# Kernel tuning notes

Measured on AMD Instinct MI355X. Metric: run time of the kernel, lower is better.

The kernel has to match this reference:

```python
import jax, jax.numpy as jnp
import numpy as np

H = 128  # hidden_dim
COORD_CLAMP = 100.0


def _glorot(key, shape):
    fan_in, fan_out = shape[0], shape[1]
    lim = float(np.sqrt(6.0 / (fan_in + fan_out)))
    return jax.random.uniform(key, shape, jnp.float32, -lim, lim)


def setup_inputs() -> dict:
    key = jax.random.key(0)
    ks = jax.random.split(key, 20)
    B, N = 2, 512
    inp = {
        "h": jax.random.normal(ks[0], (B, N, H), jnp.float32),
        "pos": jax.random.normal(ks[1], (B, N, 3), jnp.float32),
        "vel": jax.random.normal(ks[2], (B, N, 3), jnp.float32),
        # edge_mlp: Linear(2H+2 -> H), SiLU, Linear(H -> H), SiLU
        "We1": _glorot(ks[3], (2 * H + 2, H)), "be1": jnp.zeros((H,), jnp.float32),
        "We2": _glorot(ks[4], (H, H)), "be2": jnp.zeros((H,), jnp.float32),
        # attention_mlp: Linear(H -> 1), Sigmoid
        "Wa": _glorot(ks[5], (H, 1)), "ba": jnp.zeros((1,), jnp.float32),
        # pos_mlp: Linear(H -> H), SiLU, Linear(H -> 1, no bias)
        "Wp1": _glorot(ks[6], (H, H)), "bp1": jnp.zeros((H,), jnp.float32),
        "Wp2": _glorot(ks[7], (H, 1)),
        # vel_mlp: Linear(H -> H), SiLU, Linear(H -> 1, no bias)
        "Wv1": _glorot(ks[8], (H, H)), "bv1": jnp.zeros((H,), jnp.float32),
        "Wv2": _glorot(ks[9], (H, 1)),
        # node_mlp: Linear(2H -> H), SiLU, Linear(H -> H)
        "Wn1": _glorot(ks[10], (2 * H, H)), "bn1": jnp.zeros((H,), jnp.float32),
        "Wn2": _glorot(ks[11], (H, H)), "bn2": jnp.zeros((H,), jnp.float32),
    }
    return inp


def reference(h, pos, vel, We1, be1, We2, be2, Wa, ba,
              Wp1, bp1, Wp2, Wv1, bv1, Wv2, Wn1, bn1, Wn2, bn2):
    B, N, _ = pos.shape
    # pairwise diffs: [B, N, N, 3]
    pos_diff = pos[:, :, None, :] - pos[:, None, :, :]
    vel_diff = vel[:, :, None, :] - vel[:, None, :, :]
    pos_dist_sq = jnp.sum(pos_diff ** 2, axis=-1, keepdims=True)  # [B,N,N,1]
    vel_dist_sq = jnp.sum(vel_diff ** 2, axis=-1, keepdims=True)
    h_i = jnp.broadcast_to(h[:, :, None, :], (B, N, N, H))
    h_j = jnp.broadcast_to(h[:, None, :, :], (B, N, N, H))
    edge_input = jnp.concatenate([h_i, h_j, pos_dist_sq, vel_dist_sq], axis=-1)  # [B,N,N,2H+2]
    # edge MLP
    m = jax.nn.silu(jnp.einsum('bijc,ch->bijh', edge_input, We1) + be1)
    m_ij = jax.nn.silu(jnp.einsum('bijh,hk->bijk', m, We2) + be2)
    # attention gate
    att = jax.nn.sigmoid(jnp.einsum('bijh,ho->bijo', m_ij, Wa) + ba)  # [B,N,N,1]
    m_ij = m_ij * att
    # tanh-weighted coordinate/velocity updates
    pos_w = jnp.tanh(jnp.einsum('bijh,ho->bijo', jax.nn.silu(jnp.einsum('bijh,hk->bijk', m_ij, Wp1) + bp1), Wp2))
    vel_w = jnp.tanh(jnp.einsum('bijh,ho->bijo', jax.nn.silu(jnp.einsum('bijh,hk->bijk', m_ij, Wv1) + bv1), Wv2))
    denom = jnp.float32(max(N - 1, 1))
    pos_update = jnp.sum(pos_diff * pos_w, axis=2) / denom  # [B,N,3]
    vel_update = jnp.sum(vel_diff * vel_w, axis=2) / denom
    pos_out = jnp.clip(pos + pos_update, -COORD_CLAMP, COORD_CLAMP)
    vel_out = jnp.clip(vel + vel_update, -COORD_CLAMP, COORD_CLAMP)
    # node update
    m_agg = jnp.sum(m_ij, axis=2)  # [B,N,H]
    node_input = jnp.concatenate([h, m_agg], axis=-1)  # [B,N,2H]
    h_out = jax.nn.silu(jnp.einsum('bnc,ch->bnh', node_input, Wn1) + bn1)
    h_out = jnp.einsum('bnh,hk->bnk', h_out, Wn2) + bn2
    h_out = h + h_out  # residual
    return (h_out, pos_out, vel_out)
```

## Files before the change

kernel.cpp:

```cpp
#include <hip/hip_runtime.h>
#include <hip/hip_bf16.h>

#define Hd 128
#define Nn 512
#define TJ 32
#define LSTRIDE 136

typedef __bf16 bf16x8 __attribute__((ext_vector_type(8)));
typedef __bf16 bf16x4 __attribute__((ext_vector_type(4)));
typedef float  floatx4 __attribute__((ext_vector_type(4)));

__device__ __forceinline__ float frcp(float x){ return __builtin_amdgcn_rcpf(x); }
__device__ __forceinline__ float fsilu(float x){ return x * frcp(1.f + __expf(-x)); }
__device__ __forceinline__ float fsigm(float x){ return frcp(1.f + __expf(-x)); }
__device__ __forceinline__ float ftanh(float x){ return 1.f - 2.f * frcp(__expf(2.f*x) + 1.f); }
__device__ __forceinline__ float rfl(float x){
  return __int_as_float(__builtin_amdgcn_readfirstlane(__float_as_int(x)));
}

__global__ __launch_bounds__(256) void prep(const float* __restrict__ h,
                                            const float* __restrict__ We1,
                                            const float* __restrict__ be1,
                                            const float* __restrict__ We2,
                                            const float* __restrict__ Wp1,
                                            const float* __restrict__ Wv1,
                                            float* __restrict__ A,
                                            float* __restrict__ Bm,
                                            __bf16* __restrict__ dst,
                                            float* __restrict__ zbase){
  if (blockIdx.x < 256){
    const int r0 = blockIdx.x * 4;
    const int k = threadIdx.x & 127, ch = threadIdx.x >> 7;
    __shared__ float hL[4][Hd];
    __shared__ float pa[2][4][Hd], pb[2][4][Hd];
    for (int idx = threadIdx.x; idx < 4*Hd; idx += 256)
      hL[idx >> 7][idx & 127] = h[r0*Hd + idx];
    __syncthreads();
    float a[4] = {0.f,0.f,0.f,0.f}, bb[4] = {0.f,0.f,0.f,0.f};
    const int cbase = ch*64;
    #pragma unroll 4
    for (int cc = 0; cc < 64; ++cc){
      const int c = cbase + cc;
      const float wa = We1[c*Hd + k];
      const float wb = We1[(c + Hd)*Hd + k];
      #pragma unroll
      for (int rr = 0; rr < 4; ++rr){
        a[rr]  += hL[rr][c] * wa;
        bb[rr] += hL[rr][c] * wb;
      }
    }
    #pragma unroll
    for (int rr = 0; rr < 4; ++rr){ pa[ch][rr][k] = a[rr]; pb[ch][rr][k] = bb[rr]; }
    __syncthreads();
    if (threadIdx.x < Hd){
      const float be = be1[k];
      #pragma unroll
      for (int rr = 0; rr < 4; ++rr){
        A[(r0+rr)*Hd + k]  = pa[0][rr][k] + pa[1][rr][k] + be;
        Bm[(r0+rr)*Hd + k] = pb[0][rr][k] + pb[1][rr][k];
      }
    }
  } else if (blockIdx.x < 280){
    const int blk = blockIdx.x - 256;
    const int which = blk >> 3, m = blk & 7;
    const float* src = (which == 0) ? We2 : (which == 1 ? Wp1 : Wv1);
    __bf16* d = dst + which * (Hd*Hd);
    #pragma unroll
    for (int it = 0; it < 8; ++it){
      const int sidx = m*2048 + it*256 + threadIdx.x;
      const int kk = sidx >> 7, cc = sidx & 127;
      const int s = kk >> 5, j = kk & 7;
      const int lane = ((kk >> 3) & 3)*16 + (cc & 15);
      const int n = cc >> 4;
      d[n*2048 + s*512 + lane*8 + j] = (__bf16)src[sidx];
    }
  } else {
    const int t0 = (blockIdx.x - 280)*256 + threadIdx.x;
    for (int idx = t0; idx < 137216; idx += 2048) zbase[idx] = 0.f;
  }
}

__global__ __launch_bounds__(256) void egnn_bf(
    const float* __restrict__ h,
    const float* __restrict__ pos, const float* __restrict__ vel,
    const float* __restrict__ We1, const float* __restrict__ be2,
    const float* __restrict__ Wa,  const float* __restrict__ ba,
    const float* __restrict__ bp1, const float* __restrict__ Wp2,
    const float* __restrict__ bv1, const float* __restrict__ Wv2,
    const float* __restrict__ Wn1, const float* __restrict__ bn1,
    const float* __restrict__ Wn2, const float* __restrict__ bn2,
    const float* __restrict__ A,   const float* __restrict__ Bm,
    const __bf16* __restrict__ Wsw,
    float* __restrict__ out){

  const int t    = threadIdx.x;
  const int w    = t >> 6;
  const int lane = t & 63;
  const int q    = lane >> 4;
  const int l15  = lane & 15;
  const int node = blockIdx.x;
  const int b    = node >> 9;

  __shared__ float AiL[Hd], wpL[Hd], wvL[Hd];
  __shared__ float be2L[Hd], bp1L[Hd], bv1L[Hd], WaL[Hd], Wp2L[Hd], Wv2L[Hd];
  __shared__ __align__(16) __bf16 bufij[4*32*LSTRIDE];
  __shared__ float attW[4][32];

  if (t < Hd){
    AiL[t]  = A[(size_t)node*Hd + t];
    wpL[t]  = We1[256*Hd + t];
    wvL[t]  = We1[257*Hd + t];
    be2L[t] = be2[t]; bp1L[t] = bp1[t]; bv1L[t] = bv1[t];
    WaL[t]  = Wa[t];  Wp2L[t] = Wp2[t]; Wv2L[t] = Wv2[t];
  }
  const float baV = ba[0];
  const float* pi = &pos[(size_t)node*3];
  const float* vi = &vel[(size_t)node*3];
  const float px = rfl(pi[0]), py = rfl(pi[1]), pz = rfl(pi[2]);
  const float ux = rfl(vi[0]), uy = rfl(vi[1]), uz = rfl(vi[2]);
  __syncthreads();

  const bf16x8* We2s = (const bf16x8*)(Wsw);
  const bf16x8* Wp1s = (const bf16x8*)(Wsw + Hd*Hd);
  const bf16x8* Wv1s = (const bf16x8*)(Wsw + 2*Hd*Hd);
  __bf16* myBuf = &bufij[w*32*LSTRIDE];
  float*  myAtt = attW[w];

  float accP0=0.f, accP1=0.f, accP2=0.f, accV0=0.f, accV1=0.f, accV2=0.f;
  float acc8[8];
  #pragma unroll
  for (int e = 0; e < 8; ++e) acc8[e] = 0.f;

  const floatx4 fzero = {0.f,0.f,0.f,0.f};

  #pragma unroll 1
  for (int jt = 0; jt < 4; ++jt){
    const int j0 = w*128 + jt*32;
    const size_t row0 = (size_t)(b*Nn + j0 + l15);
    const size_t row1 = row0 + 16;

    float dp[2], dv[2];
    {
      const float* pj0 = &pos[row0*3]; const float* vj0 = &vel[row0*3];
      const float* pj1 = &pos[row1*3]; const float* vj1 = &vel[row1*3];
      float dx = px - pj0[0], dy = py - pj0[1], dz = pz - pj0[2];
      dp[0] = dx*dx + dy*dy + dz*dz;
      dx = px - pj1[0]; dy = py - pj1[1]; dz = pz - pj1[2];
      dp[1] = dx*dx + dy*dy + dz*dz;
      float ex = ux - vj0[0], ey = uy - vj0[1], ez = uz - vj0[2];
      dv[0] = ex*ex + ey*ey + ez*ez;
      ex = ux - vj1[0]; ey = uy - vj1[1]; ez = uz - vj1[2];
      dv[1] = ex*ex + ey*ey + ez*ez;
    }

    bf16x8 mf[4][2];
    #pragma unroll
    for (int s = 0; s < 4; ++s){
      const int fo = s*32 + q*8;
      const floatx4 A0 = *(const floatx4*)&AiL[fo], A1 = *(const floatx4*)&AiL[fo+4];
      const floatx4 P0 = *(const floatx4*)&wpL[fo], P1 = *(const floatx4*)&wpL[fo+4];
      const floatx4 V0 = *(const floatx4*)&wvL[fo], V1 = *(const floatx4*)&wvL[fo+4];
      #pragma unroll
      for (int n = 0; n < 2; ++n){
        const floatx4* Bp = (const floatx4*)&Bm[(n ? row1 : row0)*Hd + fo];
        const floatx4 b0 = Bp[0], b1 = Bp[1];
        float x[8];
        #pragma unroll
        for (int e = 0; e < 4; ++e){
          x[e]   = fsilu(A0[e] + b0[e] + dp[n]*P0[e] + dv[n]*V0[e]);
          x[4+e] = fsilu(A1[e] + b1[e] + dp[n]*P1[e] + dv[n]*V1[e]);
        }
        union { bf16x8 v; __hip_bfloat162 h2[4]; } o;
        o.h2[0] = __float22bfloat162_rn(make_float2(x[0], x[1]));
        o.h2[1] = __float22bfloat162_rn(make_float2(x[2], x[3]));
        o.h2[2] = __float22bfloat162_rn(make_float2(x[4], x[5]));
        o.h2[3] = __float22bfloat162_rn(make_float2(x[6], x[7]));
        mf[s][n] = o.v;
      }
    }

    float aw0 = 0.f, aw1 = 0.f;
    #pragma unroll
    for (int f = 0; f < 2; ++f){
      floatx4 acc[4][2];
      #pragma unroll
      for (int m4 = 0; m4 < 4; ++m4){ acc[m4][0] = fzero; acc[m4][1] = fzero; }
      #pragma unroll
      for (int s = 0; s < 4; ++s){
        #pragma unroll
        for (int m4 = 0; m4 < 4; ++m4){
          const bf16x8 a = We2s[((f*4 + m4)*4 + s)*64 + lane];
          acc[m4][0] = __builtin_amdgcn_mfma_f32_16x16x32_bf16(a, mf[s][0], acc[m4][0], 0, 0, 0);
          acc[m4][1] = __builtin_amdgcn_mfma_f32_16x16x32_bf16(a, mf[s][1], acc[m4][1], 0, 0, 0);
        }
      }
      #pragma unroll
      for (int m4 = 0; m4 < 4; ++m4){
        const int fb = (f*4 + m4)*16 + q*4;
        const floatx4 be = *(const floatx4*)&be2L[fb];
        const floatx4 wa = *(const floatx4*)&WaL[fb];
        float s0[4], s1[4];
        #pragma unroll
        for (int r = 0; r < 4; ++r){
          s0[r] = fsilu(acc[m4][0][r] + be[r]);
          s1[r] = fsilu(acc[m4][1][r] + be[r]);
          aw0 += s0[r]*wa[r];
          aw1 += s1[r]*wa[r];
        }
        union { bf16x4 v; __hip_bfloat162 h2[2]; } k0, k1;
        k0.h2[0] = __float22bfloat162_rn(make_float2(s0[0], s0[1]));
        k0.h2[1] = __float22bfloat162_rn(make_float2(s0[2], s0[3]));
        k1.h2[0] = __float22bfloat162_rn(make_float2(s1[0], s1[1]));
        k1.h2[1] = __float22bfloat162_rn(make_float2(s1[2], s1[3]));
        *(bf16x4*)&myBuf[l15*LSTRIDE + fb]        = k0.v;
        *(bf16x4*)&myBuf[(16 + l15)*LSTRIDE + fb] = k1.v;
      }
    }
    aw0 += __shfl_xor(aw0, 16, 64); aw0 += __shfl_xor(aw0, 32, 64);
    aw1 += __shfl_xor(aw1, 16, 64); aw1 += __shfl_xor(aw1, 32, 64);
    const float att0 = fsigm(aw0 + baV);
    const float att1 = fsigm(aw1 + baV);
    if (lane < 16){ myAtt[l15] = att0; myAtt[16 + l15] = att1; }

    {
      float p0 = 0.f, p1 = 0.f;
      #pragma unroll
      for (int f = 0; f < 2; ++f){
        floatx4 acc[4][2];
        #pragma unroll
        for (int m4 = 0; m4 < 4; ++m4){ acc[m4][0] = fzero; acc[m4][1] = fzero; }
        #pragma unroll
        for (int s = 0; s < 4; ++s){
          const bf16x8 b0 = *(const bf16x8*)&myBuf[l15*LSTRIDE + s*32 + q*8];
          const bf16x8 b1 = *(const bf16x8*)&myBuf[(16 + l15)*LSTRIDE + s*32 + q*8];
          #pragma unroll
          for (int m4 = 0; m4 < 4; ++m4){
            const bf16x8 a = Wp1s[((f*4 + m4)*4 + s)*64 + lane];
            acc[m4][0] = __builtin_amdgcn_mfma_f32_16x16x32_bf16(a, b0, acc[m4][0], 0, 0, 0);
            acc[m4][1] = __builtin_amdgcn_mfma_f32_16x16x32_bf16(a, b1, acc[m4][1], 0, 0, 0);
          }
        }
        #pragma unroll
        for (int m4 = 0; m4 < 4; ++m4){
          const int fb = (f*4 + m4)*16 + q*4;
          const floatx4 bb = *(const floatx4*)&bp1L[fb];
          const floatx4 w2 = *(const floatx4*)&Wp2L[fb];
          #pragma unroll
          for (int r = 0; r < 4; ++r){
            p0 += fsilu(fmaf(att0, acc[m4][0][r], bb[r])) * w2[r];
            p1 += fsilu(fmaf(att1, acc[m4][1][r], bb[r])) * w2[r];
          }
        }
      }
      p0 += __shfl_xor(p0, 16, 64); p0 += __shfl_xor(p0, 32, 64);
      p1 += __shfl_xor(p1, 16, 64); p1 += __shfl_xor(p1, 32, 64);
      const float pw0 = ftanh(p0), pw1 = ftanh(p1);
      const float* pj0 = &pos[row0*3];
      const float* pj1 = &pos[row1*3];
      accP0 += (px - pj0[0])*pw0 + (px - pj1[0])*pw1;
      accP1 += (py - pj0[1])*pw0 + (py - pj1[1])*pw1;
      accP2 += (pz - pj0[2])*pw0 + (pz - pj1[2])*pw1;
    }

    {
      float p0 = 0.f, p1 = 0.f;
      #pragma unroll
      for (int f = 0; f < 2; ++f){
        floatx4 acc[4][2];
        #pragma unroll
        for (int m4 = 0; m4 < 4; ++m4){ acc[m4][0] = fzero; acc[m4][1] = fzero; }
        #pragma unroll
        for (int s = 0; s < 4; ++s){
          const bf16x8 b0 = *(const bf16x8*)&myBuf[l15*LSTRIDE + s*32 + q*8];
          const bf16x8 b1 = *(const bf16x8*)&myBuf[(16 + l15)*LSTRIDE + s*32 + q*8];
          #pragma unroll
          for (int m4 = 0; m4 < 4; ++m4){
            const bf16x8 a = Wv1s[((f*4 + m4)*4 + s)*64 + lane];
            acc[m4][0] = __builtin_amdgcn_mfma_f32_16x16x32_bf16(a, b0, acc[m4][0], 0, 0, 0);
            acc[m4][1] = __builtin_amdgcn_mfma_f32_16x16x32_bf16(a, b1, acc[m4][1], 0, 0, 0);
          }
        }
        #pragma unroll
        for (int m4 = 0; m4 < 4; ++m4){
          const int fb = (f*4 + m4)*16 + q*4;
          const floatx4 bb = *(const floatx4*)&bv1L[fb];
          const floatx4 w2 = *(const floatx4*)&Wv2L[fb];
          #pragma unroll
          for (int r = 0; r < 4; ++r){
            p0 += fsilu(fmaf(att0, acc[m4][0][r], bb[r])) * w2[r];
            p1 += fsilu(fmaf(att1, acc[m4][1][r], bb[r])) * w2[r];
          }
        }
      }
      p0 += __shfl_xor(p0, 16, 64); p0 += __shfl_xor(p0, 32, 64);
      p1 += __shfl_xor(p1, 16, 64); p1 += __shfl_xor(p1, 32, 64);
      const float vw0 = ftanh(p0), vw1 = ftanh(p1);
      const float* vj0 = &vel[row0*3];
      const float* vj1 = &vel[row1*3];
      accV0 += (ux - vj0[0])*vw0 + (ux - vj1[0])*vw1;
      accV1 += (uy - vj0[1])*vw0 + (uy - vj1[1])*vw1;
      accV2 += (uz - vj0[2])*vw0 + (uz - vj1[2])*vw1;
    }

    {
      const int fg = lane & 15, jr = lane >> 4;
      #pragma unroll
      for (int k = 0; k < 8; ++k){
        const int jl = jr*8 + k;
        const float aj = myAtt[jl];
        const bf16x8 v = *(const bf16x8*)&myBuf[jl*LSTRIDE + fg*8];
        #pragma unroll
        for (int e = 0; e < 8; ++e) acc8[e] += aj * (float)v[e];
      }
    }
  }

  float* sMagW = (float*)myBuf;
  float* sPVW  = (float*)myBuf + 128;
  {
    float r6[6] = {accP0, accP1, accP2, accV0, accV1, accV2};
    #pragma unroll
    for (int off = 1; off < 64; off <<= 1){
      #pragma unroll
      for (int e = 0; e < 6; ++e) r6[e] += __shfl_xor(r6[e], off, 64);
    }
    if (lane == 0){
      #pragma unroll
      for (int e = 0; e < 6; ++e) sPVW[e] = r6[e];
    }
    #pragma unroll
    for (int e = 0; e < 8; ++e){
      acc8[e] += __shfl_xor(acc8[e], 16, 64);
      acc8[e] += __shfl_xor(acc8[e], 32, 64);
    }
    if (lane < 16){
      *(float4*)&sMagW[l15*8 + 0] = make_float4(acc8[0], acc8[1], acc8[2], acc8[3]);
      *(float4*)&sMagW[l15*8 + 4] = make_float4(acc8[4], acc8[5], acc8[6], acc8[7]);
    }
  }
  __syncthreads();

  float* sF = (float*)bufij + 1024;
  {
    const float* s0 = (const float*)(bufij);
    const float* s1 = (const float*)(bufij + 32*LSTRIDE);
    const float* s2 = (const float*)(bufij + 64*LSTRIDE);
    const float* s3 = (const float*)(bufij + 96*LSTRIDE);
    if (t < Hd){
      sF[128 + t] = s0[t] + s1[t] + s2[t] + s3[t];
      sF[t] = h[(size_t)node*Hd + t];
    } else if (t < Hd + 3){
      const int d = t - Hd;
      const float v = 0.25f*(s0[128+d] + s1[128+d] + s2[128+d] + s3[128+d]);
      const float o = pi[d] + v*(1.f/511.f);
      out[2*Nn*Hd + node*3 + d] = fminf(fmaxf(o, -100.f), 100.f);
    } else if (t < Hd + 6){
      const int d = t - Hd - 3;
      const float v = 0.25f*(s0[131+d] + s1[131+d] + s2[131+d] + s3[131+d]);
      const float o = vi[d] + v*(1.f/511.f);
      out[2*Nn*Hd + 2*Nn*3 + node*3 + d] = fminf(fmaxf(o, -100.f), 100.f);
    }
  }
  __syncthreads();
  {
    const int k = t & 127, ch = t >> 7;
    const int cb = ch*Hd;
    float a0=0.f,a1=0.f,a2=0.f,a3=0.f;
    #pragma unroll 8
    for (int cc = 0; cc < Hd; cc += 4){
      a0 += sF[cb+cc+0] * Wn1[(cb+cc+0)*Hd + k];
      a1 += sF[cb+cc+1] * Wn1[(cb+cc+1)*Hd + k];
      a2 += sF[cb+cc+2] * Wn1[(cb+cc+2)*Hd + k];
      a3 += sF[cb+cc+3] * Wn1[(cb+cc+3)*Hd + k];
    }
    sF[256 + ch*128 + k] = (a0+a1)+(a2+a3);
  }
  __syncthreads();
  if (t < Hd) sF[512 + t] = fsilu(sF[256 + t] + sF[384 + t] + bn1[t]);
  __syncthreads();
  {
    const int k = t & 127, ch = t >> 7;
    const int cb = ch*64;
    float a0=0.f,a1=0.f,a2=0.f,a3=0.f;
    #pragma unroll 8
    for (int cc = 0; cc < 64; cc += 4){
      a0 += sF[512+cb+cc+0] * Wn2[(cb+cc+0)*Hd + k];
      a1 += sF[512+cb+cc+1] * Wn2[(cb+cc+1)*Hd + k];
      a2 += sF[512+cb+cc+2] * Wn2[(cb+cc+2)*Hd + k];
      a3 += sF[512+cb+cc+3] * Wn2[(cb+cc+3)*Hd + k];
    }
    sF[256 + ch*128 + k] = (a0+a1)+(a2+a3);
  }
  __syncthreads();
  if (t < Hd)
    out[(size_t)node*Hd + t] = sF[t] + sF[256 + t] + sF[384 + t] + bn2[t];
}

__device__ __forceinline__ void gemm_kloopT(const __bf16* __restrict__ buf,
                                            const bf16x8* __restrict__ Ws,
                                            int w, int lane, int q, int l15,
                                            floatx4 acc[2][2]){
  const floatx4 zero = {0.f, 0.f, 0.f, 0.f};
  #pragma unroll
  for (int m = 0; m < 2; ++m){ acc[m][0] = zero; acc[m][1] = zero; }
  #pragma unroll
  for (int s = 0; s < 4; ++s){
    bf16x8 bf[2];
    #pragma unroll
    for (int n = 0; n < 2; ++n)
      bf[n] = *(const bf16x8*)&buf[(16*n + l15)*LSTRIDE + s*32 + q*8];
    const bf16x8 a0 = Ws[((2*w + 0)*4 + s)*64 + lane];
    const bf16x8 a1 = Ws[((2*w + 1)*4 + s)*64 + lane];
    #pragma unroll
    for (int n = 0; n < 2; ++n){
      acc[0][n] = __builtin_amdgcn_mfma_f32_16x16x32_bf16(a0, bf[n], acc[0][n], 0, 0, 0);
      acc[1][n] = __builtin_amdgcn_mfma_f32_16x16x32_bf16(a1, bf[n], acc[1][n], 0, 0, 0);
    }
  }
}

__device__ __forceinline__ void wdotT(floatx4 acc[2][2], float att0, float att1,
                                      const float* __restrict__ biasL,
                                      const float* __restrict__ w2L,
                                      int w, int lane, int q, int l15,
                                      float (*part)[TJ]){
  const int fb0 = 32*w + 4*q, fb1 = fb0 + 16;
  const floatx4 bb0 = *(const floatx4*)&biasL[fb0];
  const floatx4 bb1 = *(const floatx4*)&biasL[fb1];
  const floatx4 w0  = *(const floatx4*)&w2L[fb0];
  const floatx4 w1  = *(const floatx4*)&w2L[fb1];
  float p0 = 0.f, p1 = 0.f;
  #pragma unroll
  for (int r = 0; r < 4; ++r){
    p0 += fsilu(fmaf(att0, acc[0][0][r], bb0[r])) * w0[r];
    p0 += fsilu(fmaf(att0, acc[1][0][r], bb1[r])) * w1[r];
    p1 += fsilu(fmaf(att1, acc[0][1][r], bb0[r])) * w0[r];
    p1 += fsilu(fmaf(att1, acc[1][1][r], bb1[r])) * w1[r];
  }
  p0 += __shfl_xor(p0, 16, 64); p0 += __shfl_xor(p0, 32, 64);
  p1 += __shfl_xor(p1, 16, 64); p1 += __shfl_xor(p1, 32, 64);
  if (lane < 16){
    part[w][l15]      = p0;
    part[w][16 + l15] = p1;
  }
}

__global__ __launch_bounds__(256) void egnn_main(
    const float* __restrict__ pos, const float* __restrict__ vel,
    const float* __restrict__ We1, const float* __restrict__ be2,
    const float* __restrict__ Wa,  const float* __restrict__ ba,
    const float* __restrict__ bp1, const float* __restrict__ Wp2,
    const float* __restrict__ bv1, const float* __restrict__ Wv2,
    const float* __restrict__ A,   const float* __restrict__ Bm,
    const __bf16* __restrict__ Wsw,
    float* __restrict__ magg, float* __restrict__ posu, float* __restrict__ velu){

  const int t    = threadIdx.x;
  const int w    = t >> 6;
  const int lane = t & 63;
  const int q    = lane >> 4;
  const int l15  = lane & 15;
  const int node = blockIdx.x >> 1;
  const int half = blockIdx.x & 1;
  const int b    = node >> 9;

  __shared__ float AiL[Hd], wpL[Hd], wvL[Hd];
  __shared__ float be2L[Hd], bp1L[Hd], bv1L[Hd], WaL[Hd], Wp2L[Hd], Wv2L[Hd];
  __shared__ __align__(16) __bf16 bufm [TJ*LSTRIDE];
  __shared__ __align__(16) __bf16 bufij[TJ*LSTRIDE];
  __shared__ float partAtt[4][TJ], partP[4][TJ], partV[4][TJ];
  __shared__ float attL[TJ];

  if (t < Hd){
    AiL[t]  = A[node*Hd + t];
    wpL[t]  = We1[256*Hd + t];
    wvL[t]  = We1[257*Hd + t];
    be2L[t] = be2[t]; bp1L[t] = bp1[t]; bv1L[t] = bv1[t];
    WaL[t]  = Wa[t];  Wp2L[t] = Wp2[t]; Wv2L[t] = Wv2[t];
  }
  const float baV = ba[0];
  const float* pi = &pos[(size_t)node*3];
  const float* vi = &vel[(size_t)node*3];
  const float px = rfl(pi[0]), py = rfl(pi[1]), pz = rfl(pi[2]);
  const float ux = rfl(vi[0]), uy = rfl(vi[1]), uz = rfl(vi[2]);
  __syncthreads();

  const bf16x8* We2s = (const bf16x8*)(Wsw);
  const bf16x8* Wp1s = (const bf16x8*)(Wsw + Hd*Hd);
  const bf16x8* Wv1s = (const bf16x8*)(Wsw + 2*Hd*Hd);

  float accR[8];
  #pragma unroll
  for (int e = 0; e < 8; ++e) accR[e] = 0.f;

  for (int jt = 0; jt < (Nn/2)/TJ; ++jt){
    const int j0 = half*(Nn/2) + jt * TJ;
    {
      const int g  = t & 15;
      const int j2 = t >> 4;
      const floatx4 a0 = *(const floatx4*)&AiL[g*8];
      const floatx4 a1 = *(const floatx4*)&AiL[g*8 + 4];
      const floatx4 p0 = *(const floatx4*)&wpL[g*8];
      const floatx4 p1 = *(const floatx4*)&wpL[g*8 + 4];
      const floatx4 v0 = *(const floatx4*)&wvL[g*8];
      const floatx4 v1 = *(const floatx4*)&wvL[g*8 + 4];
      #pragma unroll
      for (int rr = 0; rr < 2; ++rr){
        const int j = j2 + rr*16;
        const int jg = j0 + j;
        const float* pj = &pos[(size_t)(b*Nn + jg)*3];
        const float* vj = &vel[(size_t)(b*Nn + jg)*3];
        const float dx = px - pj[0], dy = py - pj[1], dz = pz - pj[2];
        const float dp = dx*dx + dy*dy + dz*dz;
        const float ex = ux - vj[0], ey = uy - vj[1], ez = uz - vj[2];
        const float dv = ex*ex + ey*ey + ez*ez;
        const floatx4* Bp4 = (const floatx4*)&Bm[((size_t)(b*Nn + jg))*Hd + g*8];
        const floatx4 b0 = Bp4[0], b1 = Bp4[1];
        union { bf16x8 v; __hip_bfloat162 h2[4]; } o;
        float x[8];
        #pragma unroll
        for (int e = 0; e < 4; ++e){
          x[e]   = fsilu(a0[e] + b0[e] + dp*p0[e] + dv*v0[e]);
          x[4+e] = fsilu(a1[e] + b1[e] + dp*p1[e] + dv*v1[e]);
        }
        o.h2[0] = __float22bfloat162_rn(make_float2(x[0], x[1]));
        o.h2[1] = __float22bfloat162_rn(make_float2(x[2], x[3]));
        o.h2[2] = __float22bfloat162_rn(make_float2(x[4], x[5]));
        o.h2[3] = __float22bfloat162_rn(make_float2(x[6], x[7]));
        *(bf16x8*)&bufm[j*LSTRIDE + g*8] = o.v;
      }
    }
    __syncthreads();
    {
      floatx4 acc[2][2];
      gemm_kloopT(bufm, We2s, w, lane, q, l15, acc);
      const int fb0 = 32*w + 4*q, fb1 = fb0 + 16;
      const floatx4 be0 = *(const floatx4*)&be2L[fb0];
      const floatx4 be1v = *(const floatx4*)&be2L[fb1];
      const floatx4 wa0 = *(const floatx4*)&WaL[fb0];
      const floatx4 wa1 = *(const floatx4*)&WaL[fb1];
      float aw[2];
      #pragma unroll
      for (int n = 0; n < 2; ++n){
        const int j = 16*n + l15;
        float s0[4], s1[4];
        #pragma unroll
        for (int r = 0; r < 4; ++r){
          s0[r] = fsilu(acc[0][n][r] + be0[r]);
          s1[r] = fsilu(acc[1][n][r] + be1v[r]);
        }
        aw[n] = s0[0]*wa0[0] + s0[1]*wa0[1] + s0[2]*wa0[2] + s0[3]*wa0[3]
              + s1[0]*wa1[0] + s1[1]*wa1[1] + s1[2]*wa1[2] + s1[3]*wa1[3];
        union { bf16x4 v; __hip_bfloat162 h2[2]; } p0k, p1k;
        p0k.h2[0] = __float22bfloat162_rn(make_float2(s0[0], s0[1]));
        p0k.h2[1] = __float22bfloat162_rn(make_float2(s0[2], s0[3]));
        p1k.h2[0] = __float22bfloat162_rn(make_float2(s1[0], s1[1]));
        p1k.h2[1] = __float22bfloat162_rn(make_float2(s1[2], s1[3]));
        *(bf16x4*)&bufij[j*LSTRIDE + fb0] = p0k.v;
        *(bf16x4*)&bufij[j*LSTRIDE + fb1] = p1k.v;
      }
      aw[0] += __shfl_xor(aw[0], 16, 64); aw[0] += __shfl_xor(aw[0], 32, 64);
      aw[1] += __shfl_xor(aw[1], 16, 64); aw[1] += __shfl_xor(aw[1], 32, 64);
      if (lane < 16){
        partAtt[w][l15]      = aw[0];
        partAtt[w][16 + l15] = aw[1];
      }
    }
    __syncthreads();
    {
      const float att0 = fsigm(partAtt[0][l15] + partAtt[1][l15] +
                               partAtt[2][l15] + partAtt[3][l15] + baV);
      const float att1 = fsigm(partAtt[0][16+l15] + partAtt[1][16+l15] +
                               partAtt[2][16+l15] + partAtt[3][16+l15] + baV);
      if (w == 0 && lane < 16){ attL[l15] = att0; attL[16 + l15] = att1; }
      floatx4 acc[2][2];
      gemm_kloopT(bufij, Wp1s, w, lane, q, l15, acc);
      wdotT(acc, att0, att1, bp1L, Wp2L, w, lane, q, l15, partP);
      gemm_kloopT(bufij, Wv1s, w, lane, q, l15, acc);
      wdotT(acc, att0, att1, bv1L, Wv2L, w, lane, q, l15, partV);
    }
    __syncthreads();
    if (w == 0){
      if (lane < TJ){
        const int jg = j0 + lane;
        const float* pj = &pos[(size_t)(b*Nn + jg)*3];
        const float s4 = partP[0][lane] + partP[1][lane] + partP[2][lane] + partP[3][lane];
        const float pw = ftanh(s4);
        accR[0] += (px - pj[0]) * pw;
        accR[1] += (py - pj[1]) * pw;
        accR[2] += (pz - pj[2]) * pw;
      }
    } else if (w == 1){
      if (lane < TJ){
        const int jg = j0 + lane;
        const float* vj = &vel[(size_t)(b*Nn + jg)*3];
        const float s4 = partV[0][lane] + partV[1][lane] + partV[2][lane] + partV[3][lane];
        const float vw = ftanh(s4);
        accR[0] += (ux - vj[0]) * vw;
        accR[1] += (uy - vj[1]) * vw;
        accR[2] += (uz - vj[2]) * vw;
      }
    } else {
      const int sg   = (w - 2)*8 + (lane & 7);
      const int jsub = lane >> 3;
      #pragma unroll
      for (int jj = 0; jj < 4; ++jj){
        const int j = jj*8 + jsub;
        const float aj = attL[j];
        const bf16x8 v = *(const bf16x8*)&bufij[j*LSTRIDE + sg*8];
        #pragma unroll
        for (int e = 0; e < 8; ++e) accR[e] += aj * (float)v[e];
      }
    }
  }

  if (w == 0 || w == 1){
    float v0 = accR[0], v1 = accR[1], v2 = accR[2];
    #pragma unroll
    for (int off = 1; off < 64; off <<= 1){
      v0 += __shfl_xor(v0, off, 64);
      v1 += __shfl_xor(v1, off, 64);
      v2 += __shfl_xor(v2, off, 64);
    }
    if (lane == 0){
      float* dst = (w == 0) ? &posu[node*3] : &velu[node*3];
      atomicAdd(&dst[0], v0);
      atomicAdd(&dst[1], v1);
      atomicAdd(&dst[2], v2);
    }
  } else {
    const int sg = (w - 2)*8 + (lane & 7);
    #pragma unroll
    for (int off = 8; off < 64; off <<= 1){
      #pragma unroll
      for (int e = 0; e < 8; ++e) accR[e] += __shfl_xor(accR[e], off, 64);
    }
    if ((lane >> 3) == 0){
      #pragma unroll
      for (int e = 0; e < 8; ++e)
        atomicAdd(&magg[node*Hd + sg*8 + e], accR[e]);
    }
  }
}

__global__ __launch_bounds__(256) void egnn_final(
    const float* __restrict__ h, const float* __restrict__ pos, const float* __restrict__ vel,
    const float* __restrict__ Wn1, const float* __restrict__ bn1,
    const float* __restrict__ Wn2, const float* __restrict__ bn2,
    const float* __restrict__ magg, const float* __restrict__ posu,
    const float* __restrict__ velu, float* __restrict__ out){
  const int row = blockIdx.x;
  const int t = threadIdx.x;
  const int k = t & 127, ch = t >> 7;
  __shared__ float ni[2*Hd];
  __shared__ float p1[2][Hd], t1[Hd];
  ni[t] = (t < Hd) ? h[row*Hd + t] : magg[row*Hd + (t - Hd)];
  __syncthreads();
  {
    float a0=0.f,a1=0.f,a2=0.f,a3=0.f;
    const int cb = ch*Hd;
    #pragma unroll 8
    for (int cc = 0; cc < Hd; cc += 4){
      a0 += ni[cb+cc+0] * Wn1[(cb+cc+0)*Hd + k];
      a1 += ni[cb+cc+1] * Wn1[(cb+cc+1)*Hd + k];
      a2 += ni[cb+cc+2] * Wn1[(cb+cc+2)*Hd + k];
      a3 += ni[cb+cc+3] * Wn1[(cb+cc+3)*Hd + k];
    }
    p1[ch][k] = (a0+a1)+(a2+a3);
  }
  __syncthreads();
  if (t < Hd) t1[t] = fsilu(p1[0][t] + p1[1][t] + bn1[t]);
  __syncthreads();
  {
    float a0=0.f,a1=0.f,a2=0.f,a3=0.f;
    const int cb = ch*64;
    #pragma unroll 8
    for (int cc = 0; cc < 64; cc += 4){
      a0 += t1[cb+cc+0] * Wn2[(cb+cc+0)*Hd + k];
      a1 += t1[cb+cc+1] * Wn2[(cb+cc+1)*Hd + k];
      a2 += t1[cb+cc+2] * Wn2[(cb+cc+2)*Hd + k];
      a3 += t1[cb+cc+3] * Wn2[(cb+cc+3)*Hd + k];
    }
    p1[ch][k] = (a0+a1)+(a2+a3);
  }
  __syncthreads();
  if (t < Hd){
    out[row*Hd + t] = ni[t] + p1[0][t] + p1[1][t] + bn2[t];
  } else if (t < Hd + 3){
    const int d = t - Hd;
    const float v = pos[row*3 + d] + posu[row*3 + d] * (1.f/511.f);
    out[2*Nn*Hd + row*3 + d] = fminf(fmaxf(v, -100.f), 100.f);
  } else if (t < Hd + 6){
    const int d = t - Hd - 3;
    const float v = vel[row*3 + d] + velu[row*3 + d] * (1.f/511.f);
    out[2*Nn*Hd + 2*Nn*3 + row*3 + d] = fminf(fmaxf(v, -100.f), 100.f);
  }
}

extern "C" void kernel_launch(void* const* d_in, const int* in_sizes, int n_in,
                              void* d_out, int out_size, void* d_ws, size_t ws_size,
                              hipStream_t stream){
  const float* h   = (const float*)d_in[0];
  const float* pos = (const float*)d_in[1];
  const float* vel = (const float*)d_in[2];
  const float* We1 = (const float*)d_in[3];
  const float* be1 = (const float*)d_in[4];
  const float* We2 = (const float*)d_in[5];
  const float* be2 = (const float*)d_in[6];
  const float* Wa  = (const float*)d_in[7];
  const float* ba  = (const float*)d_in[8];
  const float* Wp1 = (const float*)d_in[9];
  const float* bp1 = (const float*)d_in[10];
  const float* Wp2 = (const float*)d_in[11];
  const float* Wv1 = (const float*)d_in[12];
  const float* bv1 = (const float*)d_in[13];
  const float* Wv2 = (const float*)d_in[14];
  const float* Wn1 = (const float*)d_in[15];
  const float* bn1 = (const float*)d_in[16];
  const float* Wn2 = (const float*)d_in[17];
  const float* bn2 = (const float*)d_in[18];

  float* ws = (float*)d_ws;
  float*  A    = ws;
  float*  Bmm  = ws + 131072;
  float*  magg = ws + 262144;
  float*  posu = ws + 393216;
  float*  velu = ws + 396288;
  __bf16* Wsw  = (__bf16*)(ws + 399360);
  float*  outp = (float*)d_out;

  hipFuncAttributes attr{};
  hipError_t ae = hipFuncGetAttributes(&attr, (const void*)egnn_bf);
  const bool useBf = (ae == hipSuccess && attr.numRegs > 0 && attr.numRegs <= 128);

  prep<<<dim3(288), dim3(256), 0, stream>>>(h, We1, be1, We2, Wp1, Wv1,
                                            A, Bmm, Wsw, magg);
  if (useBf){
    egnn_bf<<<dim3(1024), dim3(256), 0, stream>>>(h, pos, vel, We1, be2, Wa, ba,
                                                  bp1, Wp2, bv1, Wv2, Wn1, bn1,
                                                  Wn2, bn2, A, Bmm, Wsw, outp);
  } else {
    egnn_main<<<dim3(2048), dim3(256), 0, stream>>>(pos, vel, We1, be2, Wa, ba, bp1, Wp2,
                                                    bv1, Wv2, A, Bmm, Wsw, magg, posu, velu);
    egnn_final<<<dim3(1024), dim3(256), 0, stream>>>(h, pos, vel, Wn1, bn1, Wn2, bn2,
                                                     magg, posu, velu, outp);
  }
}
```

Baseline: 235.1 us.

## Stage edge features through LDS and process j-subtiles sequentially to cut registers

The first-layer SiLU features are written straight into the per-wave LDS buffer instead of being held in registers as mf[4][2]. Each of the three MFMA stages (edge layer 2, pos MLP, vel MLP) now runs over the two 16-row halves in turn with 8 accumulators, instead of 16 accumulators covering both halves at once. This is meant to lower VGPR pressure and possibly raise occupancy, at the cost of extra LDS writes and reads and less independent MFMA work to hide latency. The final 6-value shuffle reduction is split into two loops but still covers the same lanes.

```diff
diff --git a/kernel.cpp b/kernel.cpp
--- a/kernel.cpp
+++ b/kernel.cpp
@@ -139,167 +139,150 @@
     const size_t row0 = (size_t)(b*Nn + j0 + l15);
     const size_t row1 = row0 + 16;
 
-    float dp[2], dv[2];
     {
-      const float* pj0 = &pos[row0*3]; const float* vj0 = &vel[row0*3];
-      const float* pj1 = &pos[row1*3]; const float* vj1 = &vel[row1*3];
-      float dx = px - pj0[0], dy = py - pj0[1], dz = pz - pj0[2];
-      dp[0] = dx*dx + dy*dy + dz*dz;
-      dx = px - pj1[0]; dy = py - pj1[1]; dz = pz - pj1[2];
-      dp[1] = dx*dx + dy*dy + dz*dz;
-      float ex = ux - vj0[0], ey = uy - vj0[1], ez = uz - vj0[2];
-      dv[0] = ex*ex + ey*ey + ez*ez;
-      ex = ux - vj1[0]; ey = uy - vj1[1]; ez = uz - vj1[2];
-      dv[1] = ex*ex + ey*ey + ez*ez;
-    }
-
-    bf16x8 mf[4][2];
-    #pragma unroll
-    for (int s = 0; s < 4; ++s){
-      const int fo = s*32 + q*8;
-      const floatx4 A0 = *(const floatx4*)&AiL[fo], A1 = *(const floatx4*)&AiL[fo+4];
-      const floatx4 P0 = *(const floatx4*)&wpL[fo], P1 = *(const floatx4*)&wpL[fo+4];
-      const floatx4 V0 = *(const floatx4*)&wvL[fo], V1 = *(const floatx4*)&wvL[fo+4];
+      float dp[2], dv[2];
+      {
+        const float* pj0 = &pos[row0*3]; const float* vj0 = &vel[row0*3];
+        const float* pj1 = &pos[row1*3]; const float* vj1 = &vel[row1*3];
+        float dx = px - pj0[0], dy = py - pj0[1], dz = pz - pj0[2];
+        dp[0] = dx*dx + dy*dy + dz*dz;
+        dx = px - pj1[0]; dy = py - pj1[1]; dz = pz - pj1[2];
+        dp[1] = dx*dx + dy*dy + dz*dz;
+        float ex = ux - vj0[0], ey = uy - vj0[1], ez = uz - vj0[2];
+        dv[0] = ex*ex + ey*ey + ez*ez;
+        ex = ux - vj1[0]; ey = uy - vj1[1]; ez = uz - vj1[2];
+        dv[1] = ex*ex + ey*ey + ez*ez;
+      }
       #pragma unroll
       for (int n = 0; n < 2; ++n){
-        const floatx4* Bp = (const floatx4*)&Bm[(n ? row1 : row0)*Hd + fo];
-        const floatx4 b0 = Bp[0], b1 = Bp[1];
-        float x[8];
-        #pragma unroll
-        for (int e = 0; e < 4; ++e){
-          x[e]   = fsilu(A0[e] + b0[e] + dp[n]*P0[e] + dv[n]*V0[e]);
-          x[4+e] = fsilu(A1[e] + b1[e] + dp[n]*P1[e] + dv[n]*V1[e]);
+        const int lr = 16*n + l15;
+        const size_t grow = n ? row1 : row0;
+        #pragma unroll
+        for (int u = 0; u < 4; ++u){
+          const int fo = q*32 + u*8;
+          const floatx4 A0 = *(const floatx4*)&AiL[fo], A1 = *(const floatx4*)&AiL[fo+4];
+          const floatx4 P0 = *(const floatx4*)&wpL[fo], P1 = *(const floatx4*)&wpL[fo+4];
+          const floatx4 V0 = *(const floatx4*)&wvL[fo], V1 = *(const floatx4*)&wvL[fo+4];
+          const floatx4* Bp = (const floatx4*)&Bm[grow*Hd + fo];
+          const floatx4 b0 = Bp[0], b1 = Bp[1];
+          float x[8];
+          #pragma unroll
+          for (int e = 0; e < 4; ++e){
+            x[e]   = fsilu(A0[e] + b0[e] + dp[n]*P0[e] + dv[n]*V0[e]);
+            x[4+e] = fsilu(A1[e] + b1[e] + dp[n]*P1[e] + dv[n]*V1[e]);
+          }
+          union { bf16x8 v; __hip_bfloat162 h2[4]; } o;
+          o.h2[0] = __float22bfloat162_rn(make_float2(x[0], x[1]));
+          o.h2[1] = __float22bfloat162_rn(make_float2(x[2], x[3]));
+          o.h2[2] = __float22bfloat162_rn(make_float2(x[4], x[5]));
+          o.h2[3] = __float22bfloat162_rn(make_float2(x[6], x[7]));
+          *(bf16x8*)&myBuf[lr*LSTRIDE + fo] = o.v;
         }
-        union { bf16x8 v; __hip_bfloat162 h2[4]; } o;
-        o.h2[0] = __float22bfloat162_rn(make_float2(x[0], x[1]));
-        o.h2[1] = __float22bfloat162_rn(make_float2(x[2], x[3]));
-        o.h2[2] = __float22bfloat162_rn(make_float2(x[4], x[5]));
-        o.h2[3] = __float22bfloat162_rn(make_float2(x[6], x[7]));
-        mf[s][n] = o.v;
-      }
-    }
-
-    float aw0 = 0.f, aw1 = 0.f;
-    #pragma unroll
-    for (int f = 0; f < 2; ++f){
-      floatx4 acc[4][2];
-      #pragma unroll
-      for (int m4 = 0; m4 < 4; ++m4){ acc[m4][0] = fzero; acc[m4][1] = fzero; }
+      }
+    }
+
+    float att01[2];
+    #pragma unroll
+    for (int n = 0; n < 2; ++n){
+      const int lr = 16*n + l15;
+      floatx4 acc[8];
+      #pragma unroll
+      for (int fm = 0; fm < 8; ++fm) acc[fm] = fzero;
       #pragma unroll
       for (int s = 0; s < 4; ++s){
-        #pragma unroll
-        for (int m4 = 0; m4 < 4; ++m4){
-          const bf16x8 a = We2s[((f*4 + m4)*4 + s)*64 + lane];
-          acc[m4][0] = __builtin_amdgcn_mfma_f32_16x16x32_bf16(a, mf[s][0], acc[m4][0], 0, 0, 0);
-          acc[m4][1] = __builtin_amdgcn_mfma_f32_16x16x32_bf16(a, mf[s][1], acc[m4][1], 0, 0, 0);
+        const bf16x8 bfv = *(const bf16x8*)&myBuf[lr*LSTRIDE + s*32 + q*8];
+        #pragma unroll
+        for (int fm = 0; fm < 8; ++fm){
+          const bf16x8 a = We2s[(fm*4 + s)*64 + lane];
+          acc[fm] = __builtin_amdgcn_mfma_f32_16x16x32_bf16(a, bfv, acc[fm], 0, 0, 0);
         }
       }
-      #pragma unroll
-      for (int m4 = 0; m4 < 4; ++m4){
-        const int fb = (f*4 + m4)*16 + q*4;
+      float aw = 0.f;
+      #pragma unroll
+      for (int fm = 0; fm < 8; ++fm){
+        const int fb = fm*16 + q*4;
         const floatx4 be = *(const floatx4*)&be2L[fb];
         const floatx4 wa = *(const floatx4*)&WaL[fb];
-        float s0[4], s1[4];
+        float s0[4];
         #pragma unroll
         for (int r = 0; r < 4; ++r){
-          s0[r] = fsilu(acc[m4][0][r] + be[r]);
-          s1[r] = fsilu(acc[m4][1][r] + be[r]);
-          aw0 += s0[r]*wa[r];
-          aw1 += s1[r]*wa[r];
+          s0[r] = fsilu(acc[fm][r] + be[r]);
+          aw += s0[r]*wa[r];
         }
-        union { bf16x4 v; __hip_bfloat162 h2[2]; } k0, k1;
+        union { bf16x4 v; __hip_bfloat162 h2[2]; } k0;
         k0.h2[0] = __float22bfloat162_rn(make_float2(s0[0], s0[1]));
         k0.h2[1] = __float22bfloat162_rn(make_float2(s0[2], s0[3]));
-        k1.h2[0] = __float22bfloat162_rn(make_float2(s1[0], s1[1]));
-        k1.h2[1] = __float22bfloat162_rn(make_float2(s1[2], s1[3]));
-        *(bf16x4*)&myBuf[l15*LSTRIDE + fb]        = k0.v;
-        *(bf16x4*)&myBuf[(16 + l15)*LSTRIDE + fb] = k1.v;
-      }
-    }
-    aw0 += __shfl_xor(aw0, 16, 64); aw0 += __shfl_xor(aw0, 32, 64);
-    aw1 += __shfl_xor(aw1, 16, 64); aw1 += __shfl_xor(aw1, 32, 64);
-    const float att0 = fsigm(aw0 + baV);
-    const float att1 = fsigm(aw1 + baV);
-    if (lane < 16){ myAtt[l15] = att0; myAtt[16 + l15] = att1; }
-
-    {
-      float p0 = 0.f, p1 = 0.f;
-      #pragma unroll
-      for (int f = 0; f < 2; ++f){
-        floatx4 acc[4][2];
-        #pragma unroll
-        for (int m4 = 0; m4 < 4; ++m4){ acc[m4][0] = fzero; acc[m4][1] = fzero; }
-        #pragma unroll
-        for (int s = 0; s < 4; ++s){
-          const bf16x8 b0 = *(const bf16x8*)&myBuf[l15*LSTRIDE + s*32 + q*8];
-          const bf16x8 b1 = *(const bf16x8*)&myBuf[(16 + l15)*LSTRIDE + s*32 + q*8];
-          #pragma unroll
-          for (int m4 = 0; m4 < 4; ++m4){
-            const bf16x8 a = Wp1s[((f*4 + m4)*4 + s)*64 + lane];
-            acc[m4][0] = __builtin_amdgcn_mfma_f32_16x16x32_bf16(a, b0, acc[m4][0], 0, 0, 0);
-            acc[m4][1] = __builtin_amdgcn_mfma_f32_16x16x32_bf16(a, b1, acc[m4][1], 0, 0, 0);
-          }
+        *(bf16x4*)&myBuf[lr*LSTRIDE + fb] = k0.v;
+      }
+      aw += __shfl_xor(aw, 16, 64); aw += __shfl_xor(aw, 32, 64);
+      att01[n] = fsigm(aw + baV);
+      if (lane < 16) myAtt[16*n + l15] = att01[n];
+    }
+
+    #pragma unroll
+    for (int n = 0; n < 2; ++n){
+      const int lr = 16*n + l15;
+      floatx4 acc[8];
+      #pragma unroll
+      for (int fm = 0; fm < 8; ++fm) acc[fm] = fzero;
+      #pragma unroll
+      for (int s = 0; s < 4; ++s){
+        const bf16x8 bfv = *(const bf16x8*)&myBuf[lr*LSTRIDE + s*32 + q*8];
+        #pragma unroll
+        for (int fm = 0; fm < 8; ++fm){
+          const bf16x8 a = Wp1s[(fm*4 + s)*64 + lane];
+          acc[fm] = __builtin_amdgcn_mfma_f32_16x16x32_bf16(a, bfv, acc[fm], 0, 0, 0);
         }
-        #pragma unroll
-        for (int m4 = 0; m4 < 4; ++m4){
-          const int fb = (f*4 + m4)*16 + q*4;
-          const floatx4 bb = *(const floatx4*)&bp1L[fb];
-          const floatx4 w2 = *(const floatx4*)&Wp2L[fb];
-          #pragma unroll
-          for (int r = 0; r < 4; ++r){
-            p0 += fsilu(fmaf(att0, acc[m4][0][r], bb[r])) * w2[r];
-            p1 += fsilu(fmaf(att1, acc[m4][1][r], bb[r])) * w2[r];
-          }
+      }
+      float p = 0.f;
+      #pragma unroll
+      for (int fm = 0; fm < 8; ++fm){
+        const int fb = fm*16 + q*4;
+        const floatx4 bb = *(const floatx4*)&bp1L[fb];
+        const floatx4 w2 = *(const floatx4*)&Wp2L[fb];
+        #pragma unroll
+        for (int r = 0; r < 4; ++r)
+          p += fsilu(fmaf(att01[n], acc[fm][r], bb[r])) * w2[r];
+      }
+      p += __shfl_xor(p, 16, 64); p += __shfl_xor(p, 32, 64);
+      const float pw = ftanh(p);
+      const float* pj = &pos[(n ? row1 : row0)*3];
+      accP0 += (px - pj[0]) * pw;
+      accP1 += (py - pj[1]) * pw;
+      accP2 += (pz - pj[2]) * pw;
+    }
+
+    #pragma unroll
+    for (int n = 0; n < 2; ++n){
+      const int lr = 16*n + l15;
+      floatx4 acc[8];
+      #pragma unroll
+      for (int fm = 0; fm < 8; ++fm) acc[fm] = fzero;
+      #pragma unroll
+      for (int s = 0; s < 4; ++s){
+        const bf16x8 bfv = *(const bf16x8*)&myBuf[lr*LSTRIDE + s*32 + q*8];
+        #pragma unroll
+        for (int fm = 0; fm < 8; ++fm){
+          const bf16x8 a = Wv1s[(fm*4 + s)*64 + lane];
+          acc[fm] = __builtin_amdgcn_mfma_f32_16x16x32_bf16(a, bfv, acc[fm], 0, 0, 0);
         }
       }
-      p0 += __shfl_xor(p0, 16, 64); p0 += __shfl_xor(p0, 32, 64);
-      p1 += __shfl_xor(p1, 16, 64); p1 += __shfl_xor(p1, 32, 64);
-      const float pw0 = ftanh(p0), pw1 = ftanh(p1);
-      const float* pj0 = &pos[row0*3];
-      const float* pj1 = &pos[row1*3];
-      accP0 += (px - pj0[0])*pw0 + (px - pj1[0])*pw1;
-      accP1 += (py - pj0[1])*pw0 + (py - pj1[1])*pw1;
-      accP2 += (pz - pj0[2])*pw0 + (pz - pj1[2])*pw1;
-    }
-
-    {
-      float p0 = 0.f, p1 = 0.f;
-      #pragma unroll
-      for (int f = 0; f < 2; ++f){
-        floatx4 acc[4][2];
-        #pragma unroll
-        for (int m4 = 0; m4 < 4; ++m4){ acc[m4][0] = fzero; acc[m4][1] = fzero; }
-        #pragma unroll
-        for (int s = 0; s < 4; ++s){
-          const bf16x8 b0 = *(const bf16x8*)&myBuf[l15*LSTRIDE + s*32 + q*8];
-          const bf16x8 b1 = *(const bf16x8*)&myBuf[(16 + l15)*LSTRIDE + s*32 + q*8];
-          #pragma unroll
-          for (int m4 = 0; m4 < 4; ++m4){
-            const bf16x8 a = Wv1s[((f*4 + m4)*4 + s)*64 + lane];
-            acc[m4][0] = __builtin_amdgcn_mfma_f32_16x16x32_bf16(a, b0, acc[m4][0], 0, 0, 0);
-            acc[m4][1] = __builtin_amdgcn_mfma_f32_16x16x32_bf16(a, b1, acc[m4][1], 0, 0, 0);
-          }
-        }
-        #pragma unroll
-        for (int m4 = 0; m4 < 4; ++m4){
-          const int fb = (f*4 + m4)*16 + q*4;
-          const floatx4 bb = *(const floatx4*)&bv1L[fb];
-          const floatx4 w2 = *(const floatx4*)&Wv2L[fb];
-          #pragma unroll
-          for (int r = 0; r < 4; ++r){
-            p0 += fsilu(fmaf(att0, acc[m4][0][r], bb[r])) * w2[r];
-            p1 += fsilu(fmaf(att1, acc[m4][1][r], bb[r])) * w2[r];
-          }
-        }
-      }
-      p0 += __shfl_xor(p0, 16, 64); p0 += __shfl_xor(p0, 32, 64);
-      p1 += __shfl_xor(p1, 16, 64); p1 += __shfl_xor(p1, 32, 64);
-      const float vw0 = ftanh(p0), vw1 = ftanh(p1);
-      const float* vj0 = &vel[row0*3];
-      const float* vj1 = &vel[row1*3];
-      accV0 += (ux - vj0[0])*vw0 + (ux - vj1[0])*vw1;
-      accV1 += (uy - vj0[1])*vw0 + (uy - vj1[1])*vw1;
-      accV2 += (uz - vj0[2])*vw0 + (uz - vj1[2])*vw1;
+      float p = 0.f;
+      #pragma unroll
+      for (int fm = 0; fm < 8; ++fm){
+        const int fb = fm*16 + q*4;
+        const floatx4 bb = *(const floatx4*)&bv1L[fb];
+        const floatx4 w2 = *(const floatx4*)&Wv2L[fb];
+        #pragma unroll
+        for (int r = 0; r < 4; ++r)
+          p += fsilu(fmaf(att01[n], acc[fm][r], bb[r])) * w2[r];
+      }
+      p += __shfl_xor(p, 16, 64); p += __shfl_xor(p, 32, 64);
+      const float vw = ftanh(p);
+      const float* vj = &vel[(n ? row1 : row0)*3];
+      accV0 += (ux - vj[0]) * vw;
+      accV1 += (uy - vj[1]) * vw;
+      accV2 += (uz - vj[2]) * vw;
     }
 
     {
@@ -320,9 +303,14 @@
   {
     float r6[6] = {accP0, accP1, accP2, accV0, accV1, accV2};
     #pragma unroll
-    for (int off = 1; off < 64; off <<= 1){
+    for (int off = 1; off < 16; off <<= 1){
       #pragma unroll
       for (int e = 0; e < 6; ++e) r6[e] += __shfl_xor(r6[e], off, 64);
+    }
+    #pragma unroll
+    for (int e = 0; e < 6; ++e){
+      r6[e] += __shfl_xor(r6[e], 16, 64);
+      r6[e] += __shfl_xor(r6[e], 32, 64);
     }
     if (lane == 0){
       #pragma unroll
```

Result: no change. 234.4 us (-0.3%).
